# Kernel tuning notes

Measured on AMD Instinct MI355X. Metric: run time of the kernel, lower is better.

## Reference

```python
import jax, jax.numpy as jnp
import numpy as np

N, E = 50000, 1600000
IN_DIM, EMBED, OUT = 512, 128, 64


def setup_inputs() -> dict:
    key = jax.random.key(0)
    k = jax.random.split(key, 8)
    x = jax.random.normal(k[0], (N, IN_DIM), dtype=jnp.float32)
    edge_index = jax.random.randint(k[1], (2, E), 0, N, dtype=jnp.int32)
    W_dense = jax.random.normal(k[2], (EMBED, IN_DIM), dtype=jnp.float32) * 0.02
    b_dense = jnp.zeros((EMBED,), dtype=jnp.float32)
    W_gat = jax.random.normal(k[3], (OUT, EMBED), dtype=jnp.float32) * 0.05
    att_src = jax.random.normal(k[4], (OUT,), dtype=jnp.float32) * 0.1
    att_dst = jax.random.normal(k[5], (OUT,), dtype=jnp.float32) * 0.1
    b_gat = jnp.zeros((OUT,), dtype=jnp.float32)
    return {"x": x, "edge_index": edge_index, "W_dense": W_dense, "b_dense": b_dense,
            "W_gat": W_gat, "att_src": att_src, "att_dst": att_dst, "b_gat": b_gat}


def reference(x, edge_index, W_dense, b_dense, W_gat, att_src, att_dst, b_gat):
    # dense -> LeakyReLU(0.01) (nn.LeakyReLU default)
    h = jax.nn.leaky_relu(x @ W_dense.T + b_dense, negative_slope=0.01)  # [N, EMBED]
    n = h.shape[0]
    # GATConv (PyG, heads=1, add_self_loops=True, negative_slope=0.2)
    loops = jnp.arange(n, dtype=edge_index.dtype)
    src = jnp.concatenate([edge_index[0], loops])
    dst = jnp.concatenate([edge_index[1], loops])
    g = h @ W_gat.T  # [N, OUT]
    a_src = g @ att_src  # [N]
    a_dst = g @ att_dst  # [N]
    e = jax.nn.leaky_relu(a_src[src] + a_dst[dst], negative_slope=0.2)  # [E+N]
    # segment softmax over destination neighborhoods (self loops guarantee non-empty)
    m = jax.ops.segment_max(e, dst, num_segments=n)
    e = jnp.exp(e - m[dst])
    denom = jax.ops.segment_sum(e, dst, num_segments=n)
    alpha = e / denom[dst]
    out = jax.ops.segment_sum(g[src] * alpha[:, None], dst, num_segments=n) + b_gat
    # original returns ([embed_x], [embed_x]); we return the single embedding tensor
    return out
```

## Files before the change

### kernel.cpp

```cpp
#include <hip/hip_runtime.h>
#include <hip/hip_fp16.h>
#include <math.h>

#define IN_DIM 512
#define EMBED 128
#define OUT_DIM 64
#define NBPAD 256
#define SEGSH 12
#define CAP_LDS 10240

typedef __attribute__((ext_vector_type(8))) short bf16x8;
typedef __attribute__((ext_vector_type(4))) float f32x4;

__device__ __forceinline__ float lrelu(float v, float s) { return v > 0.f ? v : v * s; }

__device__ __forceinline__ float readlane_f(float v, int l) {
  return __int_as_float(__builtin_amdgcn_readlane(__float_as_int(v), l));
}

__device__ __forceinline__ unsigned short f2bf(float f) {
  unsigned int u = __float_as_uint(f);
  u += 0x7fff + ((u >> 16) & 1);
  return (unsigned short)(u >> 16);
}
__device__ __forceinline__ float bf2f(unsigned short h) {
  return __uint_as_float(((unsigned int)h) << 16);
}

__device__ __forceinline__ unsigned int cvt_pk_bf16(float a, float b) {
  unsigned int r;
  asm("v_cvt_pk_bf16_f32 %0, %1, %2" : "=v"(r) : "v"(a), "v"(b));
  return r;
}

__device__ __forceinline__ void gl_lds16(const void* g, void* l) {
  __builtin_amdgcn_global_load_lds(
      (const __attribute__((address_space(1))) unsigned int*)g,
      (__attribute__((address_space(3))) unsigned int*)l, 16, 0, 0);
}

__global__ __launch_bounds__(256) void split_w_kernel(
    const float* __restrict__ Wd, unsigned short* __restrict__ Wdh,
    unsigned short* __restrict__ Wdl, const float* __restrict__ Wg,
    unsigned short* __restrict__ Wgh, unsigned short* __restrict__ Wgl) {
  int i = (blockIdx.x * 256 + threadIdx.x) * 4;
  const float* W;
  unsigned short *Wh, *Wl;
  int base;
  if (i < EMBED * IN_DIM) {
    W = Wd; Wh = Wdh; Wl = Wdl; base = i;
  } else {
    base = i - EMBED * IN_DIM;
    if (base >= OUT_DIM * EMBED) return;
    W = Wg; Wh = Wgh; Wl = Wgl;
  }
  float4 v = *(const float4*)(W + base);
  unsigned int h0 = cvt_pk_bf16(v.x, v.y);
  unsigned int h1 = cvt_pk_bf16(v.z, v.w);
  float r0 = v.x - __uint_as_float(h0 << 16);
  float r1 = v.y - __uint_as_float(h0 & 0xffff0000u);
  float r2 = v.z - __uint_as_float(h1 << 16);
  float r3 = v.w - __uint_as_float(h1 & 0xffff0000u);
  unsigned int l0 = cvt_pk_bf16(r0, r1);
  unsigned int l1 = cvt_pk_bf16(r2, r3);
  *(uint2*)(Wh + base) = make_uint2(h0, h1);
  *(uint2*)(Wl + base) = make_uint2(l0, l1);
}

__global__ __launch_bounds__(256) void gemm12_fused_kernel(
    const float* __restrict__ x, const unsigned short* __restrict__ Wdh,
    const unsigned short* __restrict__ Wdl, const float* __restrict__ bd,
    const unsigned short* __restrict__ Wgh, const unsigned short* __restrict__ Wgl,
    const float* __restrict__ att_src, const float* __restrict__ att_dst,
    __half* __restrict__ gh, float* __restrict__ a_src,
    float* __restrict__ a_dst, int N) {
  __shared__ __align__(16) unsigned char SMEM[65536];

  const int tid = threadIdx.x;
  const int lane = tid & 63;
  const int wid = tid >> 6;
  const int mblk = blockIdx.x * 128;
  const int quad = lane >> 4;
  const int l15 = lane & 15;

  const float* aptr[2];
#pragma unroll
  for (int mi = 0; mi < 2; ++mi) {
    int rg = mblk + wid * 32 + mi * 16 + l15;
    if (rg >= N) rg = N - 1;
    aptr[mi] = x + (size_t)rg * IN_DIM + quad * 8;
  }
  float4 tc[2][2];
  auto loadA = [&](int k0) {
#pragma unroll
    for (int mi = 0; mi < 2; ++mi) {
      tc[mi][0] = *(const float4*)(aptr[mi] + k0);
      tc[mi][1] = *(const float4*)(aptr[mi] + k0 + 4);
    }
  };

  const char* bsrcH[2];
  const char* bsrcL[2];
  int bdst[2];
#pragma unroll
  for (int i = 0; i < 2; ++i) {
    int chunk = i * 256 + tid;
    int row = chunk >> 2, ch = chunk & 3;
    int cs = ch ^ ((row >> 1) & 3);
    size_t srcoff = (size_t)row * (IN_DIM * 2) + (cs << 4);
    bsrcH[i] = (const char*)Wdh + srcoff;
    bsrcL[i] = (const char*)Wdl + srcoff;
    bdst[i] = chunk * 16;
  }
  auto stageB = [&](int buf, int k0) {
    const size_t kb = (size_t)k0 * 2;
#pragma unroll
    for (int i = 0; i < 2; ++i) {
      gl_lds16(bsrcH[i] + kb, SMEM + buf * 8192 + bdst[i]);
      gl_lds16(bsrcL[i] + kb, SMEM + 16384 + buf * 8192 + bdst[i]);
    }
  };

  int boff[8];
#pragma unroll
  for (int ni = 0; ni < 8; ++ni) {
    int row = ni * 16 + l15;
    boff[ni] = row * 64 + ((quad ^ ((row >> 1) & 3)) << 4);
  }

  f32x4 acc[2][8];
#pragma unroll
  for (int i = 0; i < 2; ++i)
#pragma unroll
    for (int j = 0; j < 8; ++j) acc[i][j] = (f32x4){0.f, 0.f, 0.f, 0.f};

#pragma unroll
  for (int i = 0; i < 4; ++i) {
    int chunk = i * 256 + tid;
    int row = chunk >> 4, ch = chunk & 15;
    size_t srcoff = (size_t)row * (EMBED * 2) + ((ch ^ (row & 15)) << 4);
    gl_lds16((const char*)Wgh + srcoff, SMEM + 32768 + chunk * 16);
    gl_lds16((const char*)Wgl + srcoff, SMEM + 49152 + chunk * 16);
  }
  stageB(0, 0);
  loadA(0);
  __syncthreads();

#pragma unroll 2
  for (int s = 0; s < IN_DIM / 32; ++s) {
    const int buf = s & 1;
    if (s + 1 < IN_DIM / 32) stageB(buf ^ 1, (s + 1) * 32);

    bf16x8 AH[2], AL[2];
#pragma unroll
    for (int mi = 0; mi < 2; ++mi) {
      float av[8] = {tc[mi][0].x, tc[mi][0].y, tc[mi][0].z, tc[mi][0].w,
                     tc[mi][1].x, tc[mi][1].y, tc[mi][1].z, tc[mi][1].w};
      union { unsigned int u[4]; bf16x8 v; } H, L;
#pragma unroll
      for (int i = 0; i < 4; ++i) {
        unsigned int hpk = cvt_pk_bf16(av[2 * i], av[2 * i + 1]);
        float q0 = av[2 * i] - __uint_as_float(hpk << 16);
        float q1 = av[2 * i + 1] - __uint_as_float(hpk & 0xffff0000u);
        H.u[i] = hpk;
        L.u[i] = cvt_pk_bf16(q0, q1);
      }
      AH[mi] = H.v;
      AL[mi] = L.v;
    }
    if (s + 1 < IN_DIM / 32) loadA((s + 1) * 32);

#pragma unroll
    for (int hf = 0; hf < 2; ++hf) {
      bf16x8 BH[4], BL[4];
#pragma unroll
      for (int j = 0; j < 4; ++j) {
        BH[j] = *(const bf16x8*)(SMEM + buf * 8192 + boff[hf * 4 + j]);
        BL[j] = *(const bf16x8*)(SMEM + 16384 + buf * 8192 + boff[hf * 4 + j]);
      }
#pragma unroll
      for (int mi = 0; mi < 2; ++mi)
#pragma unroll
        for (int j = 0; j < 4; ++j) {
          int ni = hf * 4 + j;
          acc[mi][ni] = __builtin_amdgcn_mfma_f32_16x16x32_bf16(AH[mi], BH[j], acc[mi][ni], 0, 0, 0);
          acc[mi][ni] = __builtin_amdgcn_mfma_f32_16x16x32_bf16(AL[mi], BH[j], acc[mi][ni], 0, 0, 0);
          acc[mi][ni] = __builtin_amdgcn_mfma_f32_16x16x32_bf16(AH[mi], BL[j], acc[mi][ni], 0, 0, 0);
        }
    }
    __syncthreads();
  }

  unsigned char* Tr = SMEM;
  const unsigned char* WgHs = SMEM + 32768;
  const unsigned char* WgLs = SMEM + 49152;

  f32x4 acc2[2][4];
#pragma unroll
  for (int i = 0; i < 2; ++i)
#pragma unroll
    for (int j = 0; j < 4; ++j) acc2[i][j] = (f32x4){0.f, 0.f, 0.f, 0.f};

#pragma unroll
  for (int mi = 0; mi < 2; ++mi) {
    __syncthreads();
#pragma unroll
    for (int ni = 0; ni < 8; ++ni) {
      int n = ni * 16 + l15;
      float b = bd[n];
#pragma unroll
      for (int r = 0; r < 4; ++r) {
        float v = lrelu(acc[mi][ni][r] + b, 0.01f);
        unsigned short hi = f2bf(v);
        unsigned short lo = f2bf(v - bf2f(hi));
        unsigned int pw = ((unsigned int)hi << 16) | lo;
        int row16 = quad * 4 + r;
        int col = ni * 16 + l15;
        int cc = col >> 2;
        int cs = cc ^ (row16 & 7);
        *(unsigned int*)(Tr + wid * 8192 + row16 * 512 + cs * 16 +
                         (col & 3) * 4) = pw;
      }
    }
    __syncthreads();
#pragma unroll
    for (int ks = 0; ks < 4; ++ks) {
      const int s7 = l15 & 7;
      const int cc0 = ks * 8 + quad * 2;
      const unsigned char* tb = Tr + wid * 8192 + l15 * 512;
      union { unsigned int u[8]; uint4 v[2]; } W_;
      W_.v[0] = *(const uint4*)(tb + ((cc0 ^ s7) << 4));
      W_.v[1] = *(const uint4*)(tb + (((cc0 + 1) ^ s7) << 4));
      union { unsigned int u[4]; bf16x8 v; } H, L;
#pragma unroll
      for (int p = 0; p < 4; ++p) {
        unsigned int wA = W_.u[2 * p], wB = W_.u[2 * p + 1];
        H.u[p] = __builtin_amdgcn_perm(wB, wA, 0x07060302u);
        L.u[p] = __builtin_amdgcn_perm(wB, wA, 0x05040100u);
      }
      bf16x8 AH2 = H.v, AL2 = L.v;
#pragma unroll
      for (int ni = 0; ni < 4; ++ni) {
        int row = ni * 16 + l15;
        int chunk = ks * 4 + quad;
        int off = row * 256 + (((chunk ^ (row & 15))) << 4);
        bf16x8 BH = *(const bf16x8*)(WgHs + off);
        bf16x8 BL = *(const bf16x8*)(WgLs + off);
        acc2[mi][ni] = __builtin_amdgcn_mfma_f32_16x16x32_bf16(AH2, BH, acc2[mi][ni], 0, 0, 0);
        acc2[mi][ni] = __builtin_amdgcn_mfma_f32_16x16x32_bf16(AL2, BH, acc2[mi][ni], 0, 0, 0);
        acc2[mi][ni] = __builtin_amdgcn_mfma_f32_16x16x32_bf16(AH2, BL, acc2[mi][ni], 0, 0, 0);
      }
    }
  }

  float as_[4], ad_[4];
#pragma unroll
  for (int ni = 0; ni < 4; ++ni) {
    int n = ni * 16 + l15;
    as_[ni] = att_src[n];
    ad_[ni] = att_dst[n];
  }
#pragma unroll
  for (int mi = 0; mi < 2; ++mi) {
#pragma unroll
    for (int r = 0; r < 4; ++r) {
      int m = mblk + wid * 32 + mi * 16 + quad * 4 + r;
      float ps = acc2[mi][0][r] * as_[0] + acc2[mi][1][r] * as_[1] +
                 acc2[mi][2][r] * as_[2] + acc2[mi][3][r] * as_[3];
      float pd = acc2[mi][0][r] * ad_[0] + acc2[mi][1][r] * ad_[1] +
                 acc2[mi][2][r] * ad_[2] + acc2[mi][3][r] * ad_[3];
#pragma unroll
      for (int d = 1; d < 16; d <<= 1) {
        ps += __shfl_xor(ps, d, 64);
        pd += __shfl_xor(pd, d, 64);
      }
      if (m < N) {
#pragma unroll
        for (int ni = 0; ni < 4; ++ni)
          gh[(size_t)m * OUT_DIM + ni * 16 + l15] = __float2half(acc2[mi][ni][r]);
        if (l15 == 0) {
          a_src[m] = ps;
          a_dst[m] = pd;
        }
      }
    }
  }
}

__global__ __launch_bounds__(256) void hist_count_kernel(
    const int* __restrict__ ei, int* __restrict__ histT, int nblkP, int E,
    int N) {
  __shared__ int cnt[NBPAD];
  const int t = threadIdx.x;
  cnt[t] = 0;
  __syncthreads();
  const int T = E + N;
  const int base = blockIdx.x << SEGSH;
#pragma unroll
  for (int q = 0; q < (1 << SEGSH) / 256; ++q) {
    int i = base + q * 256 + t;
    if (i < T) {
      int d = (i < E) ? ei[E + i] : (i - E);
      atomicAdd(&cnt[d >> 8], 1);
    }
  }
  __syncthreads();
  histT[(size_t)t * nblkP + blockIdx.x] = cnt[t];
}

__global__ __launch_bounds__(256) void row_scan_kernel(
    int* __restrict__ histT, int* __restrict__ bucket_tot, int nblkP) {
  __shared__ int sc[256];
  const int t = threadIdx.x;
  int* row = histT + (size_t)blockIdx.x * nblkP;
  const int per = (nblkP + 255) / 256;
  int loc[8];
  int sum = 0;
#pragma unroll 4
  for (int j = 0; j < per; ++j) {
    int idx = t * per + j;
    int v = (idx < nblkP) ? row[idx] : 0;
    loc[j] = sum;
    sum += v;
  }
  sc[t] = sum;
  __syncthreads();
  for (int dlt = 1; dlt < 256; dlt <<= 1) {
    int add = (t >= dlt) ? sc[t - dlt] : 0;
    __syncthreads();
    sc[t] += add;
    __syncthreads();
  }
  const int off = sc[t] - sum;
#pragma unroll 4
  for (int j = 0; j < per; ++j) {
    int idx = t * per + j;
    if (idx < nblkP) row[idx] = off + loc[j];
  }
  if (t == 255) bucket_tot[blockIdx.x] = sc[255];
}

__global__ __launch_bounds__(256) void base_scan_kernel(
    const int* __restrict__ bucket_tot, int* __restrict__ bucket_base,
    int* __restrict__ offsets, int N, int T) {
  __shared__ int sc[256];
  const int t = threadIdx.x;
  int v = bucket_tot[t];
  sc[t] = v;
  __syncthreads();
  for (int dlt = 1; dlt < 256; dlt <<= 1) {
    int add = (t >= dlt) ? sc[t - dlt] : 0;
    __syncthreads();
    sc[t] += add;
    __syncthreads();
  }
  bucket_base[t] = sc[t] - v;
  if (t == 0) offsets[N] = T;
}

__global__ __launch_bounds__(256) void bin_kernel(
    const int* __restrict__ ei, const int* __restrict__ histT,
    const int* __restrict__ bucket_base, int* __restrict__ stageB, int nblkP,
    int E, int N) {
  __shared__ int cnt[NBPAD];
  __shared__ int basev[NBPAD];
  const int t = threadIdx.x;
  cnt[t] = 0;
  basev[t] = bucket_base[t] + histT[(size_t)t * nblkP + blockIdx.x];
  __syncthreads();
  const int T = E + N;
  const int base = blockIdx.x << SEGSH;
#pragma unroll
  for (int q = 0; q < (1 << SEGSH) / 256; ++q) {
    int i = base + q * 256 + t;
    if (i < T) {
      int s, d;
      if (i < E) {
        s = ei[i];
        d = ei[E + i];
      } else {
        s = d = i - E;
      }
      int b = d >> 8;
      int r = atomicAdd(&cnt[b], 1);
      stageB[basev[b] + r] = (s << 8) | (d & 255);
    }
  }
}

__global__ __launch_bounds__(256) void build_kernel(
    const int* __restrict__ stageB, const int* __restrict__ bucket_base,
    const int* __restrict__ bucket_tot, const float* __restrict__ a_src,
    const float* __restrict__ a_dst, int* __restrict__ offsets,
    int2* __restrict__ csr_pack, int N) {
  __shared__ int cnt[256];
  __shared__ int pre[256];
  __shared__ int cur[256];
  __shared__ int2 buf[CAP_LDS];
  const int b = blockIdx.x;
  const int t = threadIdx.x;
  const int base = bucket_base[b];
  const int tot = bucket_tot[b];
  cnt[t] = 0;
  __syncthreads();
  const int* sp = stageB + base;
  for (int i = t; i < tot; i += 256) atomicAdd(&cnt[sp[i] & 255], 1);
  __syncthreads();
  int v = cnt[t];
  pre[t] = v;
  __syncthreads();
  for (int dlt = 1; dlt < 256; dlt <<= 1) {
    int add = (t >= dlt) ? pre[t - dlt] : 0;
    __syncthreads();
    pre[t] += add;
    __syncthreads();
  }
  const int excl = pre[t] - v;
  cur[t] = excl;
  const int d_self = (b << 8) | t;
  if (d_self < N) offsets[d_self] = base + excl;
  __syncthreads();
  for (int i = t; i < tot; i += 256) {
    int rec = sp[i];
    int dl = rec & 255;
    int s = rec >> 8;
    float e = a_src[s] + a_dst[(b << 8) | dl];
    e = e > 0.f ? e : 0.2f * e;
    int pos = atomicAdd(&cur[dl], 1);
    int2 r2 = make_int2(s, __float_as_int(e));
    if (pos < CAP_LDS)
      buf[pos] = r2;
    else
      csr_pack[base + pos] = r2;
  }
  __syncthreads();
  const int lim = min(tot, CAP_LDS);
  for (int i = t; i < lim; i += 256) csr_pack[base + i] = buf[i];
}

__global__ __launch_bounds__(256) void aggregate_kernel(
    const int* __restrict__ offsets, const int2* __restrict__ csr_pack,
    const __half* __restrict__ gh, const float* __restrict__ b_gat,
    float* __restrict__ out, int N) {
  const int lane = threadIdx.x & 63;
  const int node = blockIdx.x * 4 + (threadIdx.x >> 6);
  if (node >= N) return;
  const int beg = offsets[node], end = offsets[node + 1];

  float m = -1e30f, l = 0.f;
  for (int j = beg + lane; j < end; j += 64) {
    float e = __int_as_float(csr_pack[j].y);
    if (e > m) {
      l = l * __expf(m - e) + 1.f;
      m = e;
    } else {
      l += __expf(e - m);
    }
  }
#pragma unroll
  for (int d = 1; d < 64; d <<= 1) {
    float mo = __shfl_xor(m, d, 64);
    float lo = __shfl_xor(l, d, 64);
    float M = fmaxf(m, mo);
    l = l * __expf(m - M) + lo * __expf(mo - M);
    m = M;
  }
  const float inv_l = 1.f / l;

  float acc0 = 0.f, acc1 = 0.f, acc2 = 0.f, acc3 = 0.f;
  for (int jb = beg; jb < end; jb += 64) {
    int j = jb + lane;
    float p = 0.f;
    int s = 0;
    if (j < end) {
      int2 rec = csr_pack[j];
      p = __expf(__int_as_float(rec.y) - m) * inv_l;
      s = rec.x;
    }
    const int cnt = min(64, end - jb);
    int jj = 0;
    for (; jj + 4 <= cnt; jj += 4) {
      int s0 = __builtin_amdgcn_readlane(s, jj);
      int s1 = __builtin_amdgcn_readlane(s, jj + 1);
      int s2 = __builtin_amdgcn_readlane(s, jj + 2);
      int s3 = __builtin_amdgcn_readlane(s, jj + 3);
      float p0 = readlane_f(p, jj);
      float p1 = readlane_f(p, jj + 1);
      float p2 = readlane_f(p, jj + 2);
      float p3 = readlane_f(p, jj + 3);
      acc0 += p0 * __half2float(gh[((size_t)s0 << 6) + lane]);
      acc1 += p1 * __half2float(gh[((size_t)s1 << 6) + lane]);
      acc2 += p2 * __half2float(gh[((size_t)s2 << 6) + lane]);
      acc3 += p3 * __half2float(gh[((size_t)s3 << 6) + lane]);
    }
    for (; jj < cnt; ++jj) {
      int s0 = __builtin_amdgcn_readlane(s, jj);
      float p0 = readlane_f(p, jj);
      acc0 += p0 * __half2float(gh[((size_t)s0 << 6) + lane]);
    }
  }
  out[(size_t)node * OUT_DIM + lane] = (acc0 + acc1) + (acc2 + acc3) + b_gat[lane];
}

extern "C" void kernel_launch(void* const* d_in, const int* in_sizes, int n_in,
                              void* d_out, int out_size, void* d_ws, size_t ws_size,
                              hipStream_t stream) {
  const float* x = (const float*)d_in[0];
  const int* ei = (const int*)d_in[1];
  const float* Wd = (const float*)d_in[2];
  const float* bd = (const float*)d_in[3];
  const float* Wg = (const float*)d_in[4];
  const float* att_src = (const float*)d_in[5];
  const float* att_dst = (const float*)d_in[6];
  const float* bg = (const float*)d_in[7];
  float* out = (float*)d_out;

  const int N = in_sizes[0] / IN_DIM;
  const int E = in_sizes[1] / 2;
  const int T = E + N;
  const int NB = (N + 255) >> 8;
  const int nblkP = (T + (1 << SEGSH) - 1) >> SEGSH;

  char* ws = (char*)d_ws;
  size_t off = 0;
  auto alloc = [&](size_t bytes) -> void* {
    void* p = ws + off;
    off += (bytes + 15) & ~(size_t)15;
    return p;
  };
  __half* gh = (__half*)alloc((size_t)N * OUT_DIM * 2);
  float* a_src = (float*)alloc((size_t)N * 4);
  float* a_dst = (float*)alloc((size_t)N * 4);
  int* offsets = (int*)alloc((size_t)(N + 1) * 4);
  int* histT = (int*)alloc((size_t)NBPAD * nblkP * 4);
  int* bucket_base = (int*)alloc((size_t)NBPAD * 4);
  int* bucket_tot = (int*)alloc((size_t)NBPAD * 4);
  int* stageB = (int*)alloc((size_t)T * 4);
  int2* csr_pack = (int2*)alloc((size_t)T * 8);
  unsigned short* Wdh = (unsigned short*)alloc((size_t)EMBED * IN_DIM * 2);
  unsigned short* Wdl = (unsigned short*)alloc((size_t)EMBED * IN_DIM * 2);
  unsigned short* Wgh = (unsigned short*)alloc((size_t)OUT_DIM * EMBED * 2);
  unsigned short* Wgl = (unsigned short*)alloc((size_t)OUT_DIM * EMBED * 2);

  const int SPLIT_TOT = EMBED * IN_DIM + OUT_DIM * EMBED;
  hipLaunchKernelGGL(split_w_kernel, dim3(SPLIT_TOT / 1024), dim3(256), 0,
                     stream, Wd, Wdh, Wdl, Wg, Wgh, Wgl);
  hipLaunchKernelGGL(gemm12_fused_kernel, dim3((N + 127) / 128), dim3(256), 0,
                     stream, x, Wdh, Wdl, bd, Wgh, Wgl, att_src, att_dst,
                     gh, a_src, a_dst, N);
  hipLaunchKernelGGL(hist_count_kernel, dim3(nblkP), dim3(256), 0, stream,
                     ei, histT, nblkP, E, N);
  hipLaunchKernelGGL(row_scan_kernel, dim3(NBPAD), dim3(256), 0, stream,
                     histT, bucket_tot, nblkP);
  hipLaunchKernelGGL(base_scan_kernel, dim3(1), dim3(256), 0, stream,
                     bucket_tot, bucket_base, offsets, N, T);
  hipLaunchKernelGGL(bin_kernel, dim3(nblkP), dim3(256), 0, stream,
                     ei, histT, bucket_base, stageB, nblkP, E, N);
  hipLaunchKernelGGL(build_kernel, dim3(NB), dim3(256), 0, stream,
                     stageB, bucket_base, bucket_tot, a_src, a_dst, offsets,
                     csr_pack, N);
  hipLaunchKernelGGL(aggregate_kernel, dim3((N + 3) / 4), dim3(256), 0, stream,
                     offsets, csr_pack, gh, bg, out, N);
}
```

Before: 295.9 us.

## Use 64-node destination buckets to raise parallelism in CSR build

Shrinks the destination bucket from 256 nodes to 64, so there are 1024 buckets instead of 256. The histogram, scans, binning and build kernels are all adapted to the new bucket count. The build kernel now launches about 782 blocks instead of 196 and needs a smaller LDS staging buffer, which should improve occupancy and load balance across CUs. In exchange the histogram matrix is four times larger, the row-scan launches four times as many blocks, and the larger per-block LDS counters in hist and bin add overhead.

```diff
diff --git a/kernel.cpp b/kernel.cpp
--- a/kernel.cpp
+++ b/kernel.cpp
@@ -5,9 +5,10 @@
 #define IN_DIM 512
 #define EMBED 128
 #define OUT_DIM 64
-#define NBPAD 256
+#define BSH 6
+#define NBKT 1024
 #define SEGSH 12
-#define CAP_LDS 10240
+#define CAP_LDS 3072
 
 typedef __attribute__((ext_vector_type(8))) short bf16x8;
 typedef __attribute__((ext_vector_type(4))) float f32x4;
@@ -290,9 +291,10 @@
 __global__ __launch_bounds__(256) void hist_count_kernel(
     const int* __restrict__ ei, int* __restrict__ histT, int nblkP, int E,
     int N) {
-  __shared__ int cnt[NBPAD];
+  __shared__ int cnt[NBKT];
   const int t = threadIdx.x;
-  cnt[t] = 0;
+#pragma unroll
+  for (int k = 0; k < NBKT / 256; ++k) cnt[k * 256 + t] = 0;
   __syncthreads();
   const int T = E + N;
   const int base = blockIdx.x << SEGSH;
@@ -301,11 +303,15 @@
     int i = base + q * 256 + t;
     if (i < T) {
       int d = (i < E) ? ei[E + i] : (i - E);
-      atomicAdd(&cnt[d >> 8], 1);
-    }
-  }
-  __syncthreads();
-  histT[(size_t)t * nblkP + blockIdx.x] = cnt[t];
+      atomicAdd(&cnt[d >> BSH], 1);
+    }
+  }
+  __syncthreads();
+#pragma unroll
+  for (int k = 0; k < NBKT / 256; ++k) {
+    int b = k * 256 + t;
+    histT[(size_t)b * nblkP + blockIdx.x] = cnt[b];
+  }
 }
 
 __global__ __launch_bounds__(256) void row_scan_kernel(
@@ -345,8 +351,15 @@
     int* __restrict__ offsets, int N, int T) {
   __shared__ int sc[256];
   const int t = threadIdx.x;
-  int v = bucket_tot[t];
-  sc[t] = v;
+  int v[4], loc[4];
+  int s4 = 0;
+#pragma unroll
+  for (int k = 0; k < 4; ++k) {
+    v[k] = bucket_tot[t * 4 + k];
+    loc[k] = s4;
+    s4 += v[k];
+  }
+  sc[t] = s4;
   __syncthreads();
   for (int dlt = 1; dlt < 256; dlt <<= 1) {
     int add = (t >= dlt) ? sc[t - dlt] : 0;
@@ -354,7 +367,9 @@
     sc[t] += add;
     __syncthreads();
   }
-  bucket_base[t] = sc[t] - v;
+  const int off = sc[t] - s4;
+#pragma unroll
+  for (int k = 0; k < 4; ++k) bucket_base[t * 4 + k] = off + loc[k];
   if (t == 0) offsets[N] = T;
 }
 
@@ -362,11 +377,15 @@
     const int* __restrict__ ei, const int* __restrict__ histT,
     const int* __restrict__ bucket_base, int* __restrict__ stageB, int nblkP,
     int E, int N) {
-  __shared__ int cnt[NBPAD];
-  __shared__ int basev[NBPAD];
+  __shared__ int cnt[NBKT];
+  __shared__ int basev[NBKT];
   const int t = threadIdx.x;
-  cnt[t] = 0;
-  basev[t] = bucket_base[t] + histT[(size_t)t * nblkP + blockIdx.x];
+#pragma unroll
+  for (int k = 0; k < NBKT / 256; ++k) {
+    int b = k * 256 + t;
+    cnt[b] = 0;
+    basev[b] = bucket_base[b] + histT[(size_t)b * nblkP + blockIdx.x];
+  }
   __syncthreads();
   const int T = E + N;
   const int base = blockIdx.x << SEGSH;
@@ -381,9 +400,9 @@
       } else {
         s = d = i - E;
       }
-      int b = d >> 8;
+      int b = d >> BSH;
       int r = atomicAdd(&cnt[b], 1);
-      stageB[basev[b] + r] = (s << 8) | (d & 255);
+      stageB[basev[b] + r] = (s << BSH) | (d & (( 1 << BSH) - 1));
     }
   }
 }
@@ -393,38 +412,43 @@
     const int* __restrict__ bucket_tot, const float* __restrict__ a_src,
     const float* __restrict__ a_dst, int* __restrict__ offsets,
     int2* __restrict__ csr_pack, int N) {
-  __shared__ int cnt[256];
-  __shared__ int pre[256];
-  __shared__ int cur[256];
+  __shared__ int cnt[64];
+  __shared__ int pre[64];
+  __shared__ int cur[64];
   __shared__ int2 buf[CAP_LDS];
   const int b = blockIdx.x;
   const int t = threadIdx.x;
   const int base = bucket_base[b];
   const int tot = bucket_tot[b];
-  cnt[t] = 0;
+  if (t < 64) cnt[t] = 0;
   __syncthreads();
   const int* sp = stageB + base;
-  for (int i = t; i < tot; i += 256) atomicAdd(&cnt[sp[i] & 255], 1);
-  __syncthreads();
-  int v = cnt[t];
-  pre[t] = v;
-  __syncthreads();
-  for (int dlt = 1; dlt < 256; dlt <<= 1) {
-    int add = (t >= dlt) ? pre[t - dlt] : 0;
-    __syncthreads();
-    pre[t] += add;
-    __syncthreads();
-  }
-  const int excl = pre[t] - v;
-  cur[t] = excl;
-  const int d_self = (b << 8) | t;
-  if (d_self < N) offsets[d_self] = base + excl;
+  for (int i = t; i < tot; i += 256) atomicAdd(&cnt[sp[i] & 63], 1);
+  __syncthreads();
+  int v = 0;
+  if (t < 64) {
+    v = cnt[t];
+    pre[t] = v;
+  }
+  __syncthreads();
+  for (int dlt = 1; dlt < 64; dlt <<= 1) {
+    int add = (t < 64 && t >= dlt) ? pre[t - dlt] : 0;
+    __syncthreads();
+    if (t < 64) pre[t] += add;
+    __syncthreads();
+  }
+  if (t < 64) {
+    int excl = pre[t] - v;
+    cur[t] = excl;
+    int d_self = (b << BSH) | t;
+    if (d_self < N) offsets[d_self] = base + excl;
+  }
   __syncthreads();
   for (int i = t; i < tot; i += 256) {
     int rec = sp[i];
-    int dl = rec & 255;
-    int s = rec >> 8;
-    float e = a_src[s] + a_dst[(b << 8) | dl];
+    int dl = rec & 63;
+    int s = rec >> BSH;
+    float e = a_src[s] + a_dst[(b << BSH) | dl];
     e = e > 0.f ? e : 0.2f * e;
     int pos = atomicAdd(&cur[dl], 1);
     int2 r2 = make_int2(s, __float_as_int(e));
@@ -518,7 +542,7 @@
   const int N = in_sizes[0] / IN_DIM;
   const int E = in_sizes[1] / 2;
   const int T = E + N;
-  const int NB = (N + 255) >> 8;
+  const int NB64 = (N + 63) >> BSH;
   const int nblkP = (T + (1 << SEGSH) - 1) >> SEGSH;
 
   char* ws = (char*)d_ws;
@@ -532,9 +556,9 @@
   float* a_src = (float*)alloc((size_t)N * 4);
   float* a_dst = (float*)alloc((size_t)N * 4);
   int* offsets = (int*)alloc((size_t)(N + 1) * 4);
-  int* histT = (int*)alloc((size_t)NBPAD * nblkP * 4);
-  int* bucket_base = (int*)alloc((size_t)NBPAD * 4);
-  int* bucket_tot = (int*)alloc((size_t)NBPAD * 4);
+  int* histT = (int*)alloc((size_t)NBKT * nblkP * 4);
+  int* bucket_base = (int*)alloc((size_t)NBKT * 4);
+  int* bucket_tot = (int*)alloc((size_t)NBKT * 4);
   int* stageB = (int*)alloc((size_t)T * 4);
   int2* csr_pack = (int2*)alloc((size_t)T * 8);
   unsigned short* Wdh = (unsigned short*)alloc((size_t)EMBED * IN_DIM * 2);
@@ -550,13 +574,13 @@
                      gh, a_src, a_dst, N);
   hipLaunchKernelGGL(hist_count_kernel, dim3(nblkP), dim3(256), 0, stream,
                      ei, histT, nblkP, E, N);
-  hipLaunchKernelGGL(row_scan_kernel, dim3(NBPAD), dim3(256), 0, stream,
+  hipLaunchKernelGGL(row_scan_kernel, dim3(NBKT), dim3(256), 0, stream,
                      histT, bucket_tot, nblkP);
   hipLaunchKernelGGL(base_scan_kernel, dim3(1), dim3(256), 0, stream,
                      bucket_tot, bucket_base, offsets, N, T);
   hipLaunchKernelGGL(bin_kernel, dim3(nblkP), dim3(256), 0, stream,
                      ei, histT, bucket_base, stageB, nblkP, E, N);
-  hipLaunchKernelGGL(build_kernel, dim3(NB), dim3(256), 0, stream,
+  hipLaunchKernelGGL(build_kernel, dim3(NB64), dim3(256), 0, stream,
                      stageB, bucket_base, bucket_tot, a_src, a_dst, offsets,
                      csr_pack, N);
   hipLaunchKernelGGL(aggregate_kernel, dim3((N + 3) / 4), dim3(256), 0, stream,
```

Measured after the change: 301.7 us. No clear change (+2.0%).
